# Performance work log

Measured on AMD Instinct MI355X. Metric: run time of the kernel, lower is better.

Reference implementation:

```python
import jax, jax.numpy as jnp
import numpy as np

B, K, C = 8192, 64, 8  # batch, feature dim, number of private-attribute classes


def setup_inputs() -> dict:
    key = jax.random.key(0)
    k1, k2, k3 = jax.random.split(key, 3)
    mu = jax.random.normal(k1, (B, K), dtype=jnp.float32)
    private_attribute = jax.random.randint(k2, (B,), 0, C)
    A = jax.random.normal(k3, (K, K), dtype=jnp.float32) * 0.05
    cov = A @ A.T + jnp.eye(K, dtype=jnp.float32)  # SPD prior covariance
    return {"mu": mu, "private_attribute": private_attribute, "cov": cov}


def _kldiv(mu1, S1, mu2, S2, k):
    # KL( N(mu1,S1) || N(mu2,S2) )
    d = mu2 - mu1
    tr = jnp.trace(jnp.linalg.solve(S2, S1))       # tr(inv(S2) S1)
    quad = d @ jnp.linalg.solve(S2, d)             # d^T inv(S2) d
    ld2 = jnp.linalg.slogdet(S2)[1]
    ld1 = jnp.linalg.slogdet(S1)[1]
    return 0.5 * (tr + quad - k + ld2 - ld1)


def reference(mu, private_attribute, cov):
    Bn, k = mu.shape
    labels = private_attribute
    ones = jnp.ones((Bn,), mu.dtype)
    counts = jax.ops.segment_sum(ones, labels, num_segments=C)                # [C]
    safe = jnp.maximum(counts, 1.0)
    mu_F = jax.ops.segment_sum(mu, labels, num_segments=C) / safe[:, None]    # [C,k] group means
    mu_total = jnp.mean(mu, axis=0)                                           # [k]
    dt = mu - mu_total
    Sigma_total = cov + dt.T @ dt / Bn                                        # [k,k]
    dc = mu - mu_F[labels]                                                    # [B,k]
    outer = jnp.einsum('bi,bj->bij', dc, dc)                                  # [B,k,k]
    Sigma_F = cov + jax.ops.segment_sum(outer, labels, num_segments=C) / safe[:, None, None]  # [C,k,k]
    kl = jax.vmap(lambda m, S: _kldiv(m, S, mu_total, Sigma_total, k))(mu_F, Sigma_F)  # [C]
    # The original loops `for i in range(len(keys)-1)` over dict keys ordered by
    # first occurrence in the batch, i.e. it SKIPS the class whose first sample
    # appears latest. Reproduce that exactly.
    pos = jnp.arange(Bn)
    first_pos = jnp.min(
        jnp.where(labels[:, None] == jnp.arange(C)[None, :], pos[:, None], Bn), axis=0
    )                                                                          # [C]
    present = first_pos < Bn
    last_key = jnp.argmax(jnp.where(present, first_pos, -1))
    w = jnp.where(present & (jnp.arange(C) != last_key), counts, 0.0)          # count_Fs weights
    result = jnp.sum(kl * w * Bn) / (Bn ** 2)
    return result
```

## Files before the change

kernel.cpp:

```cpp
#include <hip/hip_runtime.h>

#define CC 8
#define KK 64
#define BB 8192
#define NCHUNK 16
#define ROWS_PER_CHUNK (BB / NCHUNK)

#define OFF_G       0
#define OFF_GSUM    294912
#define OFF_GCOUNT  296960
#define OFF_GFIRST  296992
#define OFF_INV     297024
#define OFF_LOG     329792
#define OFF_GPART   329864

__device__ __forceinline__ double readlane_f64(double v, int lane) {
  union { double d; int i[2]; } u, r;
  u.d = v;
  r.i[0] = __builtin_amdgcn_readlane(u.i[0], lane);
  r.i[1] = __builtin_amdgcn_readlane(u.i[1], lane);
  return r.d;
}

__global__ __launch_bounds__(256) void gram_stats_kernel(
    const float* __restrict__ mu, const int* __restrict__ labels,
    float* __restrict__ Gpart, float* __restrict__ gsum,
    int* __restrict__ gcount, int* __restrict__ gfirst) {
  int c = blockIdx.y;
  int chunk = blockIdx.x;
  int tid = threadIdx.x;
  int lane = tid & 63, w = tid >> 6;
  int tx = tid & 15, ty = tid >> 4;
  __shared__ float rows[64][KK];
  __shared__ int labs[64];
  __shared__ float ssum[KK];
  double acc[4][4] = {{0.0}};
  float rsum = 0.f;
  int cnt = 0, first = BB;
  int base = chunk * ROWS_PER_CHUNK;
  const float4* mu4 = (const float4*)mu + (size_t)base * (KK / 4);

  if (tid < KK) ssum[tid] = 0.f;

  float4 pf[4];
  int plab = 0;
#pragma unroll
  for (int i = 0; i < 4; ++i) pf[i] = mu4[tid + i * 256];
  if (tid < 64) plab = labels[base + tid];

#pragma unroll 1
  for (int g = 0; g < ROWS_PER_CHUNK / 64; ++g) {
    __syncthreads();
    float4* rows4 = (float4*)&rows[0][0];
#pragma unroll
    for (int i = 0; i < 4; ++i) rows4[tid + i * 256] = pf[i];
    if (tid < 64) labs[tid] = plab;
    __syncthreads();
    if (g + 1 < ROWS_PER_CHUNK / 64) {
#pragma unroll
      for (int i = 0; i < 4; ++i) pf[i] = mu4[(g + 1) * 1024 + tid + i * 256];
      if (tid < 64) plab = labels[base + (g + 1) * 64 + tid];
    }
#pragma unroll 4
    for (int r = 0; r < 16; ++r) {
      int rr = w * 16 + r;
      if (labs[rr] == c) rsum += rows[rr][lane];
    }
    if (lane < 16 && labs[w * 16 + lane] == c) {
      cnt++;
      first = min(first, base + g * 64 + w * 16 + lane);
    }
    unsigned long long m = __ballot(labs[lane] == c);
    while (m) {
      int r = __builtin_ctzll(m);
      m &= m - 1;
      const float4* rw4 = (const float4*)rows[r];
      float4 a4 = rw4[ty], b4 = rw4[tx];
      const float* ai = (const float*)&a4;
      const float* bj = (const float*)&b4;
#pragma unroll
      for (int a = 0; a < 4; ++a)
#pragma unroll
        for (int b = 0; b < 4; ++b) acc[a][b] += (double)ai[a] * (double)bj[b];
    }
  }
  float* Gp = Gpart + ((size_t)chunk * CC + c) * KK * KK;
#pragma unroll
  for (int a = 0; a < 4; ++a)
#pragma unroll
    for (int b = 0; b < 4; ++b)
      Gp[(ty * 4 + a) * KK + tx * 4 + b] = (float)acc[a][b];
  atomicAdd(&ssum[lane], rsum);
  __syncthreads();
  if (tid < KK) {
    float v = ssum[tid];
    if (v != 0.f) atomicAdd(&gsum[c * KK + tid], v);
  }
  if (lane < 16) {
#pragma unroll
    for (int off = 8; off; off >>= 1) {
      cnt += __shfl_down(cnt, off);
      first = min(first, __shfl_down(first, off));
    }
    if (lane == 0 && cnt) {
      atomicAdd(&gcount[c], cnt);
      atomicMin(&gfirst[c], first);
    }
  }
}

__global__ __launch_bounds__(256) void greduce_kernel(
    const float* __restrict__ Gpart, double* __restrict__ G) {
  int c = blockIdx.y;
  int e = blockIdx.x * 256 + threadIdx.x;
  double s = 0.0;
  if (c < CC) {
#pragma unroll
    for (int p = 0; p < NCHUNK; ++p)
      s += (double)Gpart[((size_t)p * CC + c) * KK * KK + e];
  } else {
#pragma unroll 4
    for (int p = 0; p < NCHUNK; ++p)
#pragma unroll
      for (int c2 = 0; c2 < CC; ++c2)
        s += (double)Gpart[((size_t)p * CC + c2) * KK * KK + e];
  }
  G[(size_t)c * KK * KK + e] = s;
}

__global__ __launch_bounds__(256) void factor_kernel(
    const double* __restrict__ G, const float* __restrict__ cov,
    const float* __restrict__ gsum, const int* __restrict__ gcount,
    double* __restrict__ logdets, double* __restrict__ invS2,
    float* __restrict__ out) {
  int blk = blockIdx.x;
  int tid = threadIdx.x;
  int t = tid & 63;
  int w = tid >> 6;
  __shared__ double bufA[KK][KK + 1];
  __shared__ double bufB[KK][KK + 1];
  __shared__ double panelb[8][KK];
  __shared__ double Lb[KK][KK + 1];
  __shared__ double Ldi[KK];
  __shared__ double mb[KK];

  bool isS2 = (blk == CC);
  if (isS2 && tid == 0) out[0] = 0.f;

  double safe, ncd, mt;
  if (!isS2) {
    int nc = gcount[blk];
    ncd = (double)nc;
    safe = nc > 0 ? ncd : 1.0;
    mt = (double)gsum[blk * KK + t] / safe;
  } else {
    ncd = (double)BB;
    safe = (double)BB;
    double s = 0.0;
#pragma unroll
    for (int c = 0; c < CC; ++c) s += (double)gsum[c * KK + t];
    mt = s / safe;
  }
  if (w == 0) mb[t] = mt;
  __syncthreads();

  {
    const double* Gc = G + (size_t)blk * KK * KK;
    double inv_safe = 1.0 / safe;
#pragma unroll 2
    for (int jj = 0; jj < 16; ++jj) {
      int j = w * 16 + jj;
      bufA[t][j] = (double)cov[j * KK + t] + (Gc[j * KK + t] - ncd * mt * mb[j]) * inv_safe;
    }
  }
  __syncthreads();

  double (*cur)[KK + 1] = bufA;
  double (*nxt)[KK + 1] = bufB;
  double ldacc = 0.0;
  int bound = t | 7;
#pragma unroll 1
  for (int p = 0; p < 8; ++p) {
    const int P0 = p * 8;
    double cc_[8];
#pragma unroll
    for (int m = 0; m < 8; ++m) cc_[m] = cur[t][P0 + m];
    double uu[8];
    double pd = 1.0;
#pragma unroll
    for (int m = 0; m < 8; ++m) {
      double akk = readlane_f64(cc_[m], P0 + m);
      pd *= akk;
      double inv;
      asm("v_rcp_f64 %0, %1" : "=v"(inv) : "v"(akk));
      inv = inv * fma(-akk, inv, 2.0);
      uu[m] = cc_[m] * inv;
      if (w == 0) {
        panelb[m][t] = cc_[m];
        if (isS2) {
          double rsv = sqrt(akk) * inv;
          Lb[t][P0 + m] = cc_[m] * rsv;
          if (t == 0) Ldi[P0 + m] = rsv;
        }
      }
#pragma unroll
      for (int mm = m + 1; mm < 8; ++mm)
        cc_[mm] -= uu[m] * readlane_f64(cc_[m], P0 + mm);
    }
    ldacc += log(pd);
    __syncthreads();
#pragma unroll 1
    for (int jb = p + 1 + w; jb < 8; jb += 4) {
      int j = jb * 8;
      if (j <= bound) {
        double aj[8];
#pragma unroll
        for (int q = 0; q < 8; ++q) aj[q] = cur[t][j + q];
#pragma unroll
        for (int m = 0; m < 8; ++m)
#pragma unroll
          for (int q = 0; q < 8; ++q)
            aj[q] -= uu[m] * panelb[m][j + q];
#pragma unroll
        for (int q = 0; q < 8; ++q) nxt[t][j + q] = aj[q];
      }
    }
    __syncthreads();
    { auto tmp = cur; cur = nxt; nxt = tmp; }
  }
  if (tid == 0) logdets[blk] = ldacc;

  if (isS2) {
    double (*Xs)[KK] = (double (*)[KK])(&bufA[0][0]);
    if (w == 0) {
#pragma unroll 1
      for (int g = 0; g < 8; ++g) {
        int I0 = g * 8;
        double sv[8];
#pragma unroll
        for (int m = 0; m < 8; ++m) sv[m] = 0.0;
#pragma unroll 2
        for (int j = 0; j < I0; ++j) {
          double xj = Xs[j][t];
#pragma unroll
          for (int m = 0; m < 8; ++m) sv[m] += Lb[I0 + m][j] * xj;
        }
#pragma unroll
        for (int m = 0; m < 8; ++m) {
          int i = I0 + m;
          double x = (((i == t) ? 1.0 : 0.0) - sv[m]) * Ldi[i];
#pragma unroll
          for (int mm = m + 1; mm < 8; ++mm) sv[mm] += Lb[I0 + mm][i] * x;
          Xs[i][t] = x;
        }
      }
    }
    __syncthreads();
#pragma unroll 1
    for (int rr = 0; rr < 16; ++rr) {
      int r = w + rr * 4;
      int k0 = r > t ? r : t;
      double s = 0.0;
#pragma unroll 2
      for (int k = k0; k < KK; ++k) s += Xs[k][r] * Xs[k][t];
      invS2[r * KK + t] = s;
    }
  }
}

__global__ __launch_bounds__(64) void combine_kernel(
    const double* __restrict__ G, const double* __restrict__ invS2,
    const double* __restrict__ logdets, const float* __restrict__ cov,
    const int* __restrict__ gcount, const int* __restrict__ gfirst,
    const float* __restrict__ gsum, float* __restrict__ out) {
  int c = blockIdx.x;
  int t = threadIdx.x;
  __shared__ double mv[KK];
  __shared__ double dv[KK];

  double mtot;
  {
    double s = 0.0;
#pragma unroll
    for (int cc2 = 0; cc2 < CC; ++cc2) s += (double)gsum[cc2 * KK + t];
    mtot = s / (double)BB;
  }
  int nc = gcount[c];
  double safe = nc > 0 ? (double)nc : 1.0;
  double mt = (double)gsum[c * KK + t] / safe;
  double dt = mtot - mt;
  mv[t] = mt;
  dv[t] = dt;

  const double* Gc = G + (size_t)c * KK * KK;
  double tg = 0.0, qm = 0.0, qd = 0.0, tic = 0.0;
#pragma unroll 4
  for (int m = 0; m < KK; ++m) {
    double w = invS2[m * KK + t];
    tic += w * (double)cov[m * KK + t];
    tg += w * Gc[m * KK + t];
    qm += w * mv[m];
    qd += w * dv[m];
  }
  qm *= mt;
  qd *= dt;
#pragma unroll
  for (int m = 32; m; m >>= 1) {
    tg += __shfl_down(tg, m);
    qm += __shfl_down(qm, m);
    qd += __shfl_down(qd, m);
    tic += __shfl_down(tic, m);
  }
  if (t == 0) {
    int best = 0;
    long long bv = -2;
    for (int cc2 = 0; cc2 < CC; ++cc2) {
      long long v = gcount[cc2] > 0 ? (long long)gfirst[cc2] : -1;
      if (v > bv) { bv = v; best = cc2; }
    }
    double tr = tic + (tg - (double)nc * qm) / safe;
    double kl = 0.5 * (tr + qd - (double)KK + logdets[CC] - logdets[c]);
    double wgt = (nc > 0 && c != best) ? (double)nc : 0.0;
    atomicAdd(out, (float)(kl * wgt / (double)BB));
  }
}

extern "C" void kernel_launch(void* const* d_in, const int* in_sizes, int n_in,
                              void* d_out, int out_size, void* d_ws, size_t ws_size,
                              hipStream_t stream) {
  (void)in_sizes; (void)n_in; (void)out_size; (void)ws_size;
  const float* mu = (const float*)d_in[0];
  const int* labels = (const int*)d_in[1];
  const float* cov = (const float*)d_in[2];
  float* out = (float*)d_out;
  char* ws = (char*)d_ws;

  double* G = (double*)(ws + OFF_G);
  float* gsum = (float*)(ws + OFF_GSUM);
  int* gcount = (int*)(ws + OFF_GCOUNT);
  int* gfirst = (int*)(ws + OFF_GFIRST);
  double* invS2 = (double*)(ws + OFF_INV);
  double* logdets = (double*)(ws + OFF_LOG);
  float* Gpart = (float*)(ws + OFF_GPART);

  hipMemsetAsync(ws + OFF_GSUM, 0, OFF_GFIRST - OFF_GSUM, stream);
  hipMemsetAsync(ws + OFF_GFIRST, 0x7f, CC * sizeof(int), stream);

  gram_stats_kernel<<<dim3(NCHUNK, CC), 256, 0, stream>>>(mu, labels, Gpart, gsum, gcount, gfirst);
  greduce_kernel<<<dim3(16, CC + 1), 256, 0, stream>>>(Gpart, G);
  factor_kernel<<<CC + 1, 256, 0, stream>>>(G, cov, gsum, gcount, logdets, invS2, out);
  combine_kernel<<<CC, 64, 0, stream>>>(G, invS2, logdets, cov, gcount, gfirst, gsum, out);
}
```

Baseline: 115.7 us.

## Fuse all stages into one cooperative kernel with grid syncs

Replaces the four kernel launches and two memsets with a single cooperative kernel that runs gram accumulation, per-class reduction plus Cholesky, total-covariance factorization and combine, separated by grid-wide syncs. Global atomics are replaced by per-block partial buffers that are reduced in the class phase. The S2 Gram matrix is now built from the per-class doubles, which serializes the total-covariance factorization after the class factorizations instead of running it in parallel. A four-kernel fallback is kept in case the cooperative launch fails.

```diff
diff --git a/kernel.cpp b/kernel.cpp
--- a/kernel.cpp
+++ b/kernel.cpp
@@ -1,18 +1,25 @@
 #include <hip/hip_runtime.h>
+#include <hip/hip_cooperative_groups.h>
 
 #define CC 8
 #define KK 64
 #define BB 8192
 #define NCHUNK 16
+#define NBLK (NCHUNK * CC)
 #define ROWS_PER_CHUNK (BB / NCHUNK)
 
-#define OFF_G       0
-#define OFF_GSUM    294912
-#define OFF_GCOUNT  296960
-#define OFF_GFIRST  296992
-#define OFF_INV     297024
-#define OFF_LOG     329792
-#define OFF_GPART   329864
+#define OFF_GPART 0
+#define OFF_SPART 2097152
+#define OFF_CPART 2129920
+#define OFF_FPART 2130432
+#define OFF_G     2130944
+#define OFF_GSUM  2393088
+#define OFF_GCNT  2395136
+#define OFF_GFST  2395168
+#define OFF_INV   2395200
+#define OFF_LOG   2427968
+
+#define SMEM_DOUBLES 13120
 
 __device__ __forceinline__ double readlane_f64(double v, int lane) {
   union { double d; int i[2]; } u, r;
@@ -22,24 +29,28 @@
   return r.d;
 }
 
-__global__ __launch_bounds__(256) void gram_stats_kernel(
-    const float* __restrict__ mu, const int* __restrict__ labels,
-    float* __restrict__ Gpart, float* __restrict__ gsum,
-    int* __restrict__ gcount, int* __restrict__ gfirst) {
-  int c = blockIdx.y;
-  int chunk = blockIdx.x;
+__device__ __forceinline__ void phase_gram(const float* __restrict__ mu,
+                                           const int* __restrict__ labels,
+                                           char* ws, double* smem, int blk) {
+  int chunk = blk >> 3, c = blk & 7;
   int tid = threadIdx.x;
   int lane = tid & 63, w = tid >> 6;
   int tx = tid & 15, ty = tid >> 4;
-  __shared__ float rows[64][KK];
-  __shared__ int labs[64];
-  __shared__ float ssum[KK];
+  float* rows = (float*)smem;
+  int* labs = (int*)(smem + 2048);
+  float* ssum = (float*)(smem + 2080);
+  int* scnt = (int*)(smem + 2112);
+  int* sfst = (int*)(smem + 2114);
+  float* Gpart = (float*)(ws + OFF_GPART);
+  float* Spart = (float*)(ws + OFF_SPART);
+  int* cpart = (int*)(ws + OFF_CPART);
+  int* fpart = (int*)(ws + OFF_FPART);
+
   double acc[4][4] = {{0.0}};
   float rsum = 0.f;
   int cnt = 0, first = BB;
   int base = chunk * ROWS_PER_CHUNK;
   const float4* mu4 = (const float4*)mu + (size_t)base * (KK / 4);
-
   if (tid < KK) ssum[tid] = 0.f;
 
   float4 pf[4];
@@ -51,7 +62,7 @@
 #pragma unroll 1
   for (int g = 0; g < ROWS_PER_CHUNK / 64; ++g) {
     __syncthreads();
-    float4* rows4 = (float4*)&rows[0][0];
+    float4* rows4 = (float4*)rows;
 #pragma unroll
     for (int i = 0; i < 4; ++i) rows4[tid + i * 256] = pf[i];
     if (tid < 64) labs[tid] = plab;
@@ -64,7 +75,7 @@
 #pragma unroll 4
     for (int r = 0; r < 16; ++r) {
       int rr = w * 16 + r;
-      if (labs[rr] == c) rsum += rows[rr][lane];
+      if (labs[rr] == c) rsum += rows[rr * KK + lane];
     }
     if (lane < 16 && labs[w * 16 + lane] == c) {
       cnt++;
@@ -74,7 +85,7 @@
     while (m) {
       int r = __builtin_ctzll(m);
       m &= m - 1;
-      const float4* rw4 = (const float4*)rows[r];
+      const float4* rw4 = (const float4*)(rows + r * KK);
       float4 a4 = rw4[ty], b4 = rw4[tx];
       const float* ai = (const float*)&a4;
       const float* bj = (const float*)&b4;
@@ -84,97 +95,37 @@
         for (int b = 0; b < 4; ++b) acc[a][b] += (double)ai[a] * (double)bj[b];
     }
   }
-  float* Gp = Gpart + ((size_t)chunk * CC + c) * KK * KK;
+  int slot = chunk * CC + c;
+  float* Gp = Gpart + (size_t)slot * KK * KK;
 #pragma unroll
   for (int a = 0; a < 4; ++a)
 #pragma unroll
     for (int b = 0; b < 4; ++b)
       Gp[(ty * 4 + a) * KK + tx * 4 + b] = (float)acc[a][b];
   atomicAdd(&ssum[lane], rsum);
-  __syncthreads();
-  if (tid < KK) {
-    float v = ssum[tid];
-    if (v != 0.f) atomicAdd(&gsum[c * KK + tid], v);
-  }
-  if (lane < 16) {
-#pragma unroll
-    for (int off = 8; off; off >>= 1) {
-      cnt += __shfl_down(cnt, off);
-      first = min(first, __shfl_down(first, off));
-    }
-    if (lane == 0 && cnt) {
-      atomicAdd(&gcount[c], cnt);
-      atomicMin(&gfirst[c], first);
-    }
-  }
-}
-
-__global__ __launch_bounds__(256) void greduce_kernel(
-    const float* __restrict__ Gpart, double* __restrict__ G) {
-  int c = blockIdx.y;
-  int e = blockIdx.x * 256 + threadIdx.x;
-  double s = 0.0;
-  if (c < CC) {
-#pragma unroll
-    for (int p = 0; p < NCHUNK; ++p)
-      s += (double)Gpart[((size_t)p * CC + c) * KK * KK + e];
-  } else {
-#pragma unroll 4
-    for (int p = 0; p < NCHUNK; ++p)
-#pragma unroll
-      for (int c2 = 0; c2 < CC; ++c2)
-        s += (double)Gpart[((size_t)p * CC + c2) * KK * KK + e];
-  }
-  G[(size_t)c * KK * KK + e] = s;
-}
-
-__global__ __launch_bounds__(256) void factor_kernel(
-    const double* __restrict__ G, const float* __restrict__ cov,
-    const float* __restrict__ gsum, const int* __restrict__ gcount,
-    double* __restrict__ logdets, double* __restrict__ invS2,
-    float* __restrict__ out) {
-  int blk = blockIdx.x;
+#pragma unroll
+  for (int off = 32; off; off >>= 1) {
+    cnt += __shfl_down(cnt, off);
+    first = min(first, __shfl_down(first, off));
+  }
+  if (lane == 0) { scnt[w] = cnt; sfst[w] = first; }
+  __syncthreads();
+  if (tid < KK) Spart[(size_t)slot * KK + tid] = ssum[tid];
+  if (tid == 0) {
+    cpart[slot] = scnt[0] + scnt[1] + scnt[2] + scnt[3];
+    fpart[slot] = min(min(sfst[0], sfst[1]), min(sfst[2], sfst[3]));
+  }
+}
+
+__device__ __forceinline__ void chol64(double* smem, bool isS2, int blk,
+                                       double* __restrict__ logdets_g) {
   int tid = threadIdx.x;
-  int t = tid & 63;
-  int w = tid >> 6;
-  __shared__ double bufA[KK][KK + 1];
-  __shared__ double bufB[KK][KK + 1];
-  __shared__ double panelb[8][KK];
-  __shared__ double Lb[KK][KK + 1];
-  __shared__ double Ldi[KK];
-  __shared__ double mb[KK];
-
-  bool isS2 = (blk == CC);
-  if (isS2 && tid == 0) out[0] = 0.f;
-
-  double safe, ncd, mt;
-  if (!isS2) {
-    int nc = gcount[blk];
-    ncd = (double)nc;
-    safe = nc > 0 ? ncd : 1.0;
-    mt = (double)gsum[blk * KK + t] / safe;
-  } else {
-    ncd = (double)BB;
-    safe = (double)BB;
-    double s = 0.0;
-#pragma unroll
-    for (int c = 0; c < CC; ++c) s += (double)gsum[c * KK + t];
-    mt = s / safe;
-  }
-  if (w == 0) mb[t] = mt;
-  __syncthreads();
-
-  {
-    const double* Gc = G + (size_t)blk * KK * KK;
-    double inv_safe = 1.0 / safe;
-#pragma unroll 2
-    for (int jj = 0; jj < 16; ++jj) {
-      int j = w * 16 + jj;
-      bufA[t][j] = (double)cov[j * KK + t] + (Gc[j * KK + t] - ncd * mt * mb[j]) * inv_safe;
-    }
-  }
-  __syncthreads();
-
+  int t = tid & 63, w = tid >> 6;
+  double (*bufA)[KK + 1] = (double (*)[KK + 1])smem;
+  double (*bufB)[KK + 1] = (double (*)[KK + 1])(smem + 4160);
+  double (*panelb)[KK] = (double (*)[KK])(smem + 8320);
+  double (*Lb)[KK + 1] = (double (*)[KK + 1])(smem + 8832);
+  double* Ldi = smem + 12992;
   double (*cur)[KK + 1] = bufA;
   double (*nxt)[KK + 1] = bufB;
   double ldacc = 0.0;
@@ -219,8 +170,7 @@
 #pragma unroll
         for (int m = 0; m < 8; ++m)
 #pragma unroll
-          for (int q = 0; q < 8; ++q)
-            aj[q] -= uu[m] * panelb[m][j + q];
+          for (int q = 0; q < 8; ++q) aj[q] -= uu[m] * panelb[m][j + q];
 #pragma unroll
         for (int q = 0; q < 8; ++q) nxt[t][j + q] = aj[q];
       }
@@ -228,63 +178,146 @@
     __syncthreads();
     { auto tmp = cur; cur = nxt; nxt = tmp; }
   }
-  if (tid == 0) logdets[blk] = ldacc;
-
-  if (isS2) {
-    double (*Xs)[KK] = (double (*)[KK])(&bufA[0][0]);
-    if (w == 0) {
-#pragma unroll 1
-      for (int g = 0; g < 8; ++g) {
-        int I0 = g * 8;
-        double sv[8];
-#pragma unroll
-        for (int m = 0; m < 8; ++m) sv[m] = 0.0;
+  if (tid == 0) logdets_g[blk] = ldacc;
+}
+
+__device__ __forceinline__ void phase_class(const float* __restrict__ cov,
+                                            char* ws, double* smem, int c) {
+  int tid = threadIdx.x;
+  float* Spart = (float*)(ws + OFF_SPART);
+  int* cpart = (int*)(ws + OFF_CPART);
+  int* fpart = (int*)(ws + OFF_FPART);
+  float* Gpart = (float*)(ws + OFF_GPART);
+  double* Gg = (double*)(ws + OFF_G);
+  float* gsum = (float*)(ws + OFF_GSUM);
+  int* gcount = (int*)(ws + OFF_GCNT);
+  int* gfirst = (int*)(ws + OFF_GFST);
+  double* mb = smem + 13056;
+  double* tmp = smem + 12992;
+
+  if (tid < KK) {
+    double s = 0.0;
+#pragma unroll
+    for (int p = 0; p < NCHUNK; ++p) s += (double)Spart[(size_t)(p * CC + c) * KK + tid];
+    gsum[c * KK + tid] = (float)s;
+    mb[tid] = s;
+  } else if (tid == 64) {
+    int ct = 0;
+#pragma unroll
+    for (int p = 0; p < NCHUNK; ++p) ct += cpart[p * CC + c];
+    gcount[c] = ct;
+    tmp[0] = (double)ct;
+  } else if (tid == 65) {
+    int ff = BB;
+#pragma unroll
+    for (int p = 0; p < NCHUNK; ++p) ff = min(ff, fpart[p * CC + c]);
+    gfirst[c] = ff;
+  }
+  __syncthreads();
+  double ncd = tmp[0];
+  double safe = ncd > 0.0 ? ncd : 1.0;
+  double inv_safe = 1.0 / safe;
+  if (tid < KK) mb[tid] *= inv_safe;
+  __syncthreads();
+
+  double (*bufA)[KK + 1] = (double (*)[KK + 1])smem;
+#pragma unroll 1
+  for (int e = tid; e < KK * KK; e += 256) {
+    double g = 0.0;
+#pragma unroll
+    for (int p = 0; p < NCHUNK; ++p) g += (double)Gpart[(size_t)(p * CC + c) * KK * KK + e];
+    Gg[(size_t)c * KK * KK + e] = g;
+    int tt = e & 63, jj = e >> 6;
+    bufA[tt][jj] = (double)cov[e] + (g - ncd * mb[tt] * mb[jj]) * inv_safe;
+  }
+  __syncthreads();
+  chol64(smem, false, c, (double*)(ws + OFF_LOG));
+}
+
+__device__ __forceinline__ void phase_total(const float* __restrict__ cov,
+                                            char* ws, double* smem) {
+  int tid = threadIdx.x;
+  int t = tid & 63, w = tid >> 6;
+  double* Gg = (double*)(ws + OFF_G);
+  float* gsum = (float*)(ws + OFF_GSUM);
+  double* mb = smem + 13056;
+
+  if (tid < KK) {
+    double s = 0.0;
+#pragma unroll
+    for (int c = 0; c < CC; ++c) s += (double)gsum[c * KK + tid];
+    mb[tid] = s / (double)BB;
+  }
+  __syncthreads();
+  double (*bufA)[KK + 1] = (double (*)[KK + 1])smem;
+  const double invB = 1.0 / (double)BB;
+#pragma unroll 1
+  for (int e = tid; e < KK * KK; e += 256) {
+    double g = 0.0;
+#pragma unroll
+    for (int c = 0; c < CC; ++c) g += Gg[(size_t)c * KK * KK + e];
+    int tt = e & 63, jj = e >> 6;
+    bufA[tt][jj] = (double)cov[e] + g * invB - mb[tt] * mb[jj];
+  }
+  __syncthreads();
+  chol64(smem, true, CC, (double*)(ws + OFF_LOG));
+
+  double (*Xs)[KK] = (double (*)[KK])smem;
+  double (*Lb)[KK + 1] = (double (*)[KK + 1])(smem + 8832);
+  double* Ldi = smem + 12992;
+  if (w == 0) {
+#pragma unroll 1
+    for (int g = 0; g < 8; ++g) {
+      int I0 = g * 8;
+      double sv[8];
+#pragma unroll
+      for (int m = 0; m < 8; ++m) sv[m] = 0.0;
 #pragma unroll 2
-        for (int j = 0; j < I0; ++j) {
-          double xj = Xs[j][t];
-#pragma unroll
-          for (int m = 0; m < 8; ++m) sv[m] += Lb[I0 + m][j] * xj;
-        }
-#pragma unroll
-        for (int m = 0; m < 8; ++m) {
-          int i = I0 + m;
-          double x = (((i == t) ? 1.0 : 0.0) - sv[m]) * Ldi[i];
-#pragma unroll
-          for (int mm = m + 1; mm < 8; ++mm) sv[mm] += Lb[I0 + mm][i] * x;
-          Xs[i][t] = x;
-        }
+      for (int j = 0; j < I0; ++j) {
+        double xj = Xs[j][t];
+#pragma unroll
+        for (int m = 0; m < 8; ++m) sv[m] += Lb[I0 + m][j] * xj;
       }
-    }
-    __syncthreads();
-#pragma unroll 1
-    for (int rr = 0; rr < 16; ++rr) {
-      int r = w + rr * 4;
-      int k0 = r > t ? r : t;
-      double s = 0.0;
+#pragma unroll
+      for (int m = 0; m < 8; ++m) {
+        int i = I0 + m;
+        double x = (((i == t) ? 1.0 : 0.0) - sv[m]) * Ldi[i];
+#pragma unroll
+        for (int mm = m + 1; mm < 8; ++mm) sv[mm] += Lb[I0 + mm][i] * x;
+        Xs[i][t] = x;
+      }
+    }
+  }
+  __syncthreads();
+  double* invS2 = (double*)(ws + OFF_INV);
+#pragma unroll 1
+  for (int rr = 0; rr < 16; ++rr) {
+    int r = w + rr * 4;
+    int k0 = r > t ? r : t;
+    double s = 0.0;
 #pragma unroll 2
-      for (int k = k0; k < KK; ++k) s += Xs[k][r] * Xs[k][t];
-      invS2[r * KK + t] = s;
-    }
-  }
-}
-
-__global__ __launch_bounds__(64) void combine_kernel(
-    const double* __restrict__ G, const double* __restrict__ invS2,
-    const double* __restrict__ logdets, const float* __restrict__ cov,
-    const int* __restrict__ gcount, const int* __restrict__ gfirst,
-    const float* __restrict__ gsum, float* __restrict__ out) {
-  int c = blockIdx.x;
+    for (int k = k0; k < KK; ++k) s += Xs[k][r] * Xs[k][t];
+    invS2[r * KK + t] = s;
+  }
+}
+
+__device__ __forceinline__ void phase_combine(const float* __restrict__ cov,
+                                              char* ws, float* out, double* smem, int c) {
   int t = threadIdx.x;
-  __shared__ double mv[KK];
-  __shared__ double dv[KK];
-
-  double mtot;
-  {
-    double s = 0.0;
-#pragma unroll
-    for (int cc2 = 0; cc2 < CC; ++cc2) s += (double)gsum[cc2 * KK + t];
-    mtot = s / (double)BB;
-  }
+  if (t >= 64) return;
+  double* Gg = (double*)(ws + OFF_G);
+  double* invS2 = (double*)(ws + OFF_INV);
+  double* logdets = (double*)(ws + OFF_LOG);
+  float* gsum = (float*)(ws + OFF_GSUM);
+  int* gcount = (int*)(ws + OFF_GCNT);
+  int* gfirst = (int*)(ws + OFF_GFST);
+  double* mv = smem;
+  double* dv = smem + 64;
+
+  double mtot = 0.0;
+#pragma unroll
+  for (int cc2 = 0; cc2 < CC; ++cc2) mtot += (double)gsum[cc2 * KK + t];
+  mtot /= (double)BB;
   int nc = gcount[c];
   double safe = nc > 0 ? (double)nc : 1.0;
   double mt = (double)gsum[c * KK + t] / safe;
@@ -292,15 +325,15 @@
   mv[t] = mt;
   dv[t] = dt;
 
-  const double* Gc = G + (size_t)c * KK * KK;
+  const double* Gc = Gg + (size_t)c * KK * KK;
   double tg = 0.0, qm = 0.0, qd = 0.0, tic = 0.0;
 #pragma unroll 4
   for (int m = 0; m < KK; ++m) {
-    double w = invS2[m * KK + t];
-    tic += w * (double)cov[m * KK + t];
-    tg += w * Gc[m * KK + t];
-    qm += w * mv[m];
-    qd += w * dv[m];
+    double w2 = invS2[m * KK + t];
+    tic += w2 * (double)cov[m * KK + t];
+    tg += w2 * Gc[m * KK + t];
+    qm += w2 * mv[m];
+    qd += w2 * dv[m];
   }
   qm *= mt;
   qd *= dt;
@@ -323,6 +356,44 @@
     double wgt = (nc > 0 && c != best) ? (double)nc : 0.0;
     atomicAdd(out, (float)(kl * wgt / (double)BB));
   }
+}
+
+__global__ void __launch_bounds__(256) fused_all(const float* __restrict__ mu,
+                                                 const int* __restrict__ labels,
+                                                 const float* __restrict__ cov,
+                                                 float* out, char* ws) {
+  __shared__ double smem[SMEM_DOUBLES];
+  cooperative_groups::grid_group grid = cooperative_groups::this_grid();
+  int blk = blockIdx.x;
+  phase_gram(mu, labels, ws, smem, blk);
+  grid.sync();
+  if (blk < CC) phase_class(cov, ws, smem, blk);
+  else if (blk == CC && threadIdx.x == 0) out[0] = 0.f;
+  grid.sync();
+  if (blk == CC) phase_total(cov, ws, smem);
+  grid.sync();
+  if (blk < CC) phase_combine(cov, ws, out, smem, blk);
+}
+
+__global__ void __launch_bounds__(256) k_gram(const float* __restrict__ mu,
+                                              const int* __restrict__ labels, char* ws) {
+  __shared__ double smem[2176];
+  phase_gram(mu, labels, ws, smem, blockIdx.x);
+}
+__global__ void __launch_bounds__(256) k_class(const float* __restrict__ cov,
+                                               float* out, char* ws) {
+  __shared__ double smem[SMEM_DOUBLES];
+  if (blockIdx.x < CC) phase_class(cov, ws, smem, blockIdx.x);
+  else if (threadIdx.x == 0) out[0] = 0.f;
+}
+__global__ void __launch_bounds__(256) k_total(const float* __restrict__ cov, char* ws) {
+  __shared__ double smem[SMEM_DOUBLES];
+  phase_total(cov, ws, smem);
+}
+__global__ void __launch_bounds__(256) k_combine(const float* __restrict__ cov,
+                                                 float* out, char* ws) {
+  __shared__ double smem[128];
+  phase_combine(cov, ws, out, smem, blockIdx.x);
 }
 
 extern "C" void kernel_launch(void* const* d_in, const int* in_sizes, int n_in,
@@ -335,19 +406,13 @@
   float* out = (float*)d_out;
   char* ws = (char*)d_ws;
 
-  double* G = (double*)(ws + OFF_G);
-  float* gsum = (float*)(ws + OFF_GSUM);
-  int* gcount = (int*)(ws + OFF_GCOUNT);
-  int* gfirst = (int*)(ws + OFF_GFIRST);
-  double* invS2 = (double*)(ws + OFF_INV);
-  double* logdets = (double*)(ws + OFF_LOG);
-  float* Gpart = (float*)(ws + OFF_GPART);
-
-  hipMemsetAsync(ws + OFF_GSUM, 0, OFF_GFIRST - OFF_GSUM, stream);
-  hipMemsetAsync(ws + OFF_GFIRST, 0x7f, CC * sizeof(int), stream);
-
-  gram_stats_kernel<<<dim3(NCHUNK, CC), 256, 0, stream>>>(mu, labels, Gpart, gsum, gcount, gfirst);
-  greduce_kernel<<<dim3(16, CC + 1), 256, 0, stream>>>(Gpart, G);
-  factor_kernel<<<CC + 1, 256, 0, stream>>>(G, cov, gsum, gcount, logdets, invS2, out);
-  combine_kernel<<<CC, 64, 0, stream>>>(G, invS2, logdets, cov, gcount, gfirst, gsum, out);
-}
+  void* args[] = {(void*)&mu, (void*)&labels, (void*)&cov, (void*)&out, (void*)&ws};
+  hipError_t err = hipLaunchCooperativeKernel(
+      reinterpret_cast<const void*>(fused_all), dim3(NBLK), dim3(256), args, 0, stream);
+  if (err != hipSuccess) {
+    k_gram<<<NBLK, 256, 0, stream>>>(mu, labels, ws);
+    k_class<<<CC + 1, 256, 0, stream>>>(cov, out, ws);
+    k_total<<<1, 256, 0, stream>>>(cov, ws);
+    k_combine<<<CC, 256, 0, stream>>>(cov, out, ws);
+  }
+}
```

Result: slower. 180.4 us (+55.9%).
